# Performance work log

Measured on AMD Instinct MI355X. Metric: run time of the kernel, lower is better.

Reference implementation:

```python
import jax, jax.numpy as jnp
import numpy as np

THETA = 10000.0
D_K = 128


def setup_inputs() -> dict:
    key = jax.random.key(0)
    k1, _ = jax.random.split(key)
    x = jax.random.normal(k1, (4, 4096, D_K), dtype=jnp.float32)
    token_positions = jnp.arange(4096, dtype=jnp.int64)
    return {"x": x, "token_positions": token_positions}


def reference(x, token_positions):
    # Original builds block-diagonal 2x2 rotation matrices R[i] with
    # angle(i,k) = i / theta**(2k/d_k) and computes R[pos] @ x.
    # That matmul is mathematically the pairwise rotation below (same values).
    d_k = x.shape[-1]
    k = jnp.arange(d_k // 2, dtype=jnp.float32)
    inv_freq = THETA ** (-2.0 * k / d_k)                 # [d_k/2]
    pos = token_positions.astype(jnp.float32)
    angles = pos[:, None] * inv_freq[None, :]            # [seq, d_k/2]
    cos = jnp.cos(angles)                                # [seq, d_k/2]
    sin = jnp.sin(angles)
    xp = x.reshape(*x.shape[:-1], d_k // 2, 2)           # [b, s, d_k/2, 2]
    xe, xo = xp[..., 0], xp[..., 1]
    oe = cos * xe - sin * xo                             # even output lanes
    oo = sin * xe + cos * xo                             # odd output lanes
    out = jnp.stack([oe, oo], axis=-1).reshape(x.shape)
    return out
```

## Files before the change

### kernel.cpp

```cpp
#include <hip/hip_runtime.h>


#define D_K 128

__global__ __launch_bounds__(256) void rope_kernel(
    const float4* __restrict__ x4,
    const int*    __restrict__ pos,
    float4*       __restrict__ out4,
    int nrow4,
    int nbatch)
{
    int i = blockIdx.x * blockDim.x + threadIdx.x;
    if (i >= nrow4) return;

    int d4 = i & (D_K / 4 - 1);
    int s  = i >> 5;

    float p_rev = (float)pos[s] * 0.15915494309189535f;

    const float L    = 0.20762050593046014f;
    const float STEP = 0.86596432336006535f;
    int   k0 = d4 << 1;
    float f0 = __builtin_amdgcn_exp2f(-L * (float)k0);
    float f1 = f0 * STEP;

    float r0 = __builtin_amdgcn_fractf(p_rev * f0);
    float r1 = __builtin_amdgcn_fractf(p_rev * f1);

    float s0 = __builtin_amdgcn_sinf(r0);
    float c0 = __builtin_amdgcn_cosf(r0);
    float s1 = __builtin_amdgcn_sinf(r1);
    float c1 = __builtin_amdgcn_cosf(r1);

    #pragma unroll 4
    for (int b = 0; b < nbatch; ++b) {
        int idx = i + b * nrow4;
        float4 v = x4[idx];
        float4 o;
        o.x = c0 * v.x - s0 * v.y;
        o.y = s0 * v.x + c0 * v.y;
        o.z = c1 * v.z - s1 * v.w;
        o.w = s1 * v.z + c1 * v.w;
        out4[idx] = o;
    }
}

extern "C" void kernel_launch(void* const* d_in, const int* in_sizes, int n_in,
                              void* d_out, int out_size, void* d_ws, size_t ws_size,
                              hipStream_t stream) {
    const float4* x4  = (const float4*)d_in[0];
    const int*    pos = (const int*)d_in[1];
    float4*       o4  = (float4*)d_out;

    int n     = in_sizes[0];
    int seq   = in_sizes[1];
    int n4    = n / 4;
    int nrow4 = seq * (D_K / 4);
    int nbatch = n4 / nrow4;

    int block = 256;
    int grid  = (nrow4 + block - 1) / block;
    rope_kernel<<<grid, block, 0, stream>>>(x4, pos, o4, nrow4, nbatch);
}
```

Baseline: 60.90 us.

## Flatten batch loop into one-element-per-thread grid with nontemporal loads/stores

Removes the per-thread loop over batches and launches one thread per float4 across all batches, so the grid is four times larger and each thread recomputes its sin/cos values. Sequence index is recovered by a mask when seq is a power of two, otherwise by modulo. Loads and stores now use nontemporal builtins to avoid polluting cache for streaming data. This trades redundant transcendental work for more memory-level parallelism.

```diff
diff --git a/kernel.cpp b/kernel.cpp
--- a/kernel.cpp
+++ b/kernel.cpp
@@ -3,18 +3,22 @@
 
 #define D_K 128
 
+typedef float vf4 __attribute__((ext_vector_type(4)));
+
+template <bool POW2>
 __global__ __launch_bounds__(256) void rope_kernel(
-    const float4* __restrict__ x4,
-    const int*    __restrict__ pos,
-    float4*       __restrict__ out4,
-    int nrow4,
-    int nbatch)
+    const vf4* __restrict__ x4,
+    const int* __restrict__ pos,
+    vf4*       __restrict__ out4,
+    int n4,
+    int seq_or_mask)
 {
     int i = blockIdx.x * blockDim.x + threadIdx.x;
-    if (i >= nrow4) return;
+    if (i >= n4) return;
 
-    int d4 = i & (D_K / 4 - 1);
-    int s  = i >> 5;
+    int d4  = i & (D_K / 4 - 1);
+    int row = i >> 5;
+    int s   = POW2 ? (row & seq_or_mask) : (row % seq_or_mask);
 
     float p_rev = (float)pos[s] * 0.15915494309189535f;
 
@@ -32,33 +36,32 @@
     float s1 = __builtin_amdgcn_sinf(r1);
     float c1 = __builtin_amdgcn_cosf(r1);
 
-    #pragma unroll 4
-    for (int b = 0; b < nbatch; ++b) {
-        int idx = i + b * nrow4;
-        float4 v = x4[idx];
-        float4 o;
-        o.x = c0 * v.x - s0 * v.y;
-        o.y = s0 * v.x + c0 * v.y;
-        o.z = c1 * v.z - s1 * v.w;
-        o.w = s1 * v.z + c1 * v.w;
-        out4[idx] = o;
-    }
+    vf4 v = __builtin_nontemporal_load(&x4[i]);
+    vf4 o;
+    o.x = c0 * v.x - s0 * v.y;
+    o.y = s0 * v.x + c0 * v.y;
+    o.z = c1 * v.z - s1 * v.w;
+    o.w = s1 * v.z + c1 * v.w;
+    __builtin_nontemporal_store(o, &out4[i]);
 }
 
 extern "C" void kernel_launch(void* const* d_in, const int* in_sizes, int n_in,
                               void* d_out, int out_size, void* d_ws, size_t ws_size,
                               hipStream_t stream) {
-    const float4* x4  = (const float4*)d_in[0];
-    const int*    pos = (const int*)d_in[1];
-    float4*       o4  = (float4*)d_out;
+    const vf4* x4  = (const vf4*)d_in[0];
+    const int* pos = (const int*)d_in[1];
+    vf4*       o4  = (vf4*)d_out;
 
-    int n     = in_sizes[0];
-    int seq   = in_sizes[1];
-    int n4    = n / 4;
-    int nrow4 = seq * (D_K / 4);
-    int nbatch = n4 / nrow4;
+    int n   = in_sizes[0];
+    int seq = in_sizes[1];
+    int n4  = n / 4;
 
     int block = 256;
-    int grid  = (nrow4 + block - 1) / block;
-    rope_kernel<<<grid, block, 0, stream>>>(x4, pos, o4, nrow4, nbatch);
+    int grid  = (n4 + block - 1) / block;
+
+    if ((seq & (seq - 1)) == 0) {
+        rope_kernel<true ><<<grid, block, 0, stream>>>(x4, pos, o4, n4, seq - 1);
+    } else {
+        rope_kernel<false><<<grid, block, 0, stream>>>(x4, pos, o4, n4, seq);
+    }
 }
```

Result: no change. 60.98 us (+0.1%).
